# Kernel optimization log

Measured on AMD Instinct MI355X. Metric: run time of the kernel, lower is better.

The kernel has to match this reference:

```python
import jax, jax.numpy as jnp
import numpy as np

B, N, E, H = 2, 2048, 512, 8
D = E // H
SCALE_BASE = 512.0
EPS = 1e-6


def _xpos_tables(n, d):
    # XPOS (torchscale): per-dim scale ramp + standard sinusoidal freqs
    half = d // 2
    xscale = (np.arange(0, d, 2, dtype=np.float32) + 0.4 * d) / (1.4 * d)  # [half]
    min_pos = -(n // 2)
    power = (np.arange(min_pos, n + min_pos, dtype=np.float32) / SCALE_BASE)[:, None]
    scale = xscale[None, :] ** power                                       # [n, half]
    inv_freq = 1.0 / (10000.0 ** (np.arange(0, half, dtype=np.float32) / half))
    sinusoid = np.arange(n, dtype=np.float32)[:, None] * inv_freq[None, :]  # [n, half]
    return (jnp.asarray(np.sin(sinusoid), jnp.float32),
            jnp.asarray(np.cos(sinusoid), jnp.float32),
            jnp.asarray(scale, jnp.float32))


def _dup_interleave(m):
    # [n, half] -> [n, d], each column repeated twice interleaved
    return jnp.repeat(m, 2, axis=-1)


def _rotate_every_two(x):
    x1, x2 = x[..., ::2], x[..., 1::2]
    return jnp.stack((-x2, x1), axis=-1).reshape(x.shape)


def _apply_xpos(x, sin, cos, scale):
    s = _dup_interleave(sin * scale)  # [n, d]
    c = _dup_interleave(cos * scale)
    return x * c + _rotate_every_two(x) * s


def _decay_mask(n, dtype=jnp.float32):
    # gammas per head: 1 - exp(linspace(log(1/32), log(1/512), H))
    gammas = 1.0 - jnp.exp(jnp.linspace(np.log(1.0 / 32), np.log(1.0 / 512), H)).astype(dtype)
    pos = jnp.arange(n, dtype=dtype)
    dist = pos[:, None] - pos[None, :]                 # [n, s]
    dist_c = jnp.where(dist >= 0, dist, 0.0)
    return jnp.where(dist[None] >= 0, gammas[:, None, None] ** dist_c[None], 0.0)  # [h, n, s]


def _msr_forward(query, key, value, Wq, bq, Wk, bk, Wv, bv, Wg, bg, Wo, bo):
    b, n, e = query.shape
    q = (query @ Wq.T + bq).reshape(b, n, H, D).transpose(0, 2, 1, 3)  # [b,h,n,d]
    k = (key   @ Wk.T + bk).reshape(b, n, H, D).transpose(0, 2, 1, 3)
    v = (value @ Wv.T + bv).reshape(b, n, H, D).transpose(0, 2, 1, 3)

    sin, cos, scale = _xpos_tables(n, D)
    q = _apply_xpos(q, sin, cos, scale)
    k = _apply_xpos(k, sin, cos, 1.0 / scale)  # downscale=True

    k = k / jnp.asarray(np.sqrt(D), q.dtype)   # scale = head_dim ** 0.5
    mask = _decay_mask(n, q.dtype)             # [h,n,s]

    sim = jnp.einsum('bhnd,bhsd->bhns', q, k) * mask[None]
    ret = jnp.einsum('bhns,bhsd->bhnd', sim, v)  # [b,h,n,d]

    # GroupNorm(groups=H, channels=H, affine=False) on [(b n), h, d]:
    # normalize each (b, n, h) slice over its d elements
    mean = ret.mean(axis=-1, keepdims=True)
    var = ret.var(axis=-1, keepdims=True)
    ret = (ret - mean) / jnp.sqrt(var + EPS)

    ret = ret.transpose(0, 2, 1, 3).reshape(b, n, e)
    gate = jax.nn.silu(query @ Wg.T + bg)
    return (ret * gate) @ Wo.T + bo


def setup_inputs() -> dict:
    key = jax.random.key(0)
    ks = jax.random.split(key, 13)
    std = float(np.sqrt(2.0 / (E + E)))  # xavier_normal for square Linear
    mk = lambda k: jax.random.normal(k, (E, E), jnp.float32) * std
    return {
        'query': jax.random.normal(ks[0], (B, N, E), jnp.float32),
        'key':   jax.random.normal(ks[1], (B, N, E), jnp.float32),
        'value': jax.random.normal(ks[2], (B, N, E), jnp.float32),
        'Wq': mk(ks[3]), 'bq': jnp.zeros((E,), jnp.float32),
        'Wk': mk(ks[4]), 'bk': jnp.zeros((E,), jnp.float32),
        'Wv': mk(ks[5]), 'bv': jnp.zeros((E,), jnp.float32),
        'Wg': mk(ks[6]), 'bg': jnp.zeros((E,), jnp.float32),
        'Wo': mk(ks[7]), 'bo': jnp.zeros((E,), jnp.float32),
    }


def reference(query, key, value, Wq, bq, Wk, bk, Wv, bv, Wg, bg, Wo, bo):
    return _msr_forward(query, key, value, Wq, bq, Wk, bk, Wv, bv, Wg, bg, Wo, bo)
```

## Files before the change

kernel.cpp:

```cpp
#include <hip/hip_runtime.h>
#include <math.h>

#define Bc 2
#define Nc 2048
#define Ec 512
#define Hc 8
#define Dc 64
#define Mc 4096
#define NT 32
#define Cc 64

typedef short bf16x8 __attribute__((ext_vector_type(8)));
typedef float f32x4 __attribute__((ext_vector_type(4)));

#define GLOAD(g, l) __builtin_amdgcn_global_load_lds(                        \
    (const __attribute__((address_space(1))) unsigned*)(const void*)(g),     \
    (__attribute__((address_space(3))) unsigned*)(void*)(l), 16, 0, 0)

#define VMCNT(n) asm volatile("s_waitcnt vmcnt(" #n ")" ::: "memory")

__device__ __forceinline__ unsigned short f2bf(float x) {
    union { float f; unsigned u; } v; v.f = x;
    unsigned r = v.u + 0x7fffu + ((v.u >> 16) & 1u);
    return (unsigned short)(r >> 16);
}
__device__ __forceinline__ float bf2f(unsigned short b) {
    union { float f; unsigned u; } v; v.u = ((unsigned)b) << 16;
    return v.f;
}

__device__ __forceinline__ float get_gamma(int h) {
    const float l0 = -3.4657359028f;
    const float l1 = -6.2383246250f;
    return 1.0f - expf(l0 + (l1 - l0) * ((float)h / 7.0f));
}

struct SplitArgs {
    const float* src[8];
    unsigned short* hi[8];
    unsigned short* lo[8];
    int n[8];
};

__global__ __launch_bounds__(256) void prep_kernel(SplitArgs a,
                                                   float* __restrict__ sinS,
                                                   float* __restrict__ cosS,
                                                   float* __restrict__ sinIS,
                                                   float* __restrict__ cosIS) {
    int y = blockIdx.y;
    if (y == 8) {
        int idx = blockIdx.x * 256 + threadIdx.x;
        if (idx >= Nc * 32) return;
        int n = idx & 2047;
        int i = idx >> 11;
        float xscale = (2.0f * (float)i + 25.6f) / 89.6f;
        float power  = ((float)n - 1024.0f) / 512.0f;
        float scale  = powf(xscale, power);
        float inv_freq = powf(10000.0f, -(float)i / 32.0f);
        float ang = (float)n * inv_freq;
        float s = sinf(ang), c = cosf(ang);
        int o = i * 2048 + n;
        sinS[o]  = s * scale;
        cosS[o]  = c * scale;
        float rs = 0.125f / scale;
        sinIS[o] = s * rs;
        cosIS[o] = c * rs;
        return;
    }
    int i4 = (blockIdx.x * 256 + threadIdx.x) * 4;
    if (i4 >= a.n[y]) return;
    float4 v = *(const float4*)&a.src[y][i4];
    ushort4 h, l;
    h.x = f2bf(v.x); l.x = f2bf(v.x - bf2f(h.x));
    h.y = f2bf(v.y); l.y = f2bf(v.y - bf2f(h.y));
    h.z = f2bf(v.z); l.z = f2bf(v.z - bf2f(h.z));
    h.w = f2bf(v.w); l.w = f2bf(v.w - bf2f(h.w));
    *(ushort4*)&a.hi[y][i4] = h;
    *(ushort4*)&a.lo[y][i4] = l;
}

template<int TM, int TN, int WR, int WC>
__global__ __launch_bounds__(WR * WC * 64) void mgemm_kernel(
    const unsigned short* __restrict__ Xq_h, const unsigned short* __restrict__ Xq_l,
    const unsigned short* __restrict__ Xk_h, const unsigned short* __restrict__ Xk_l,
    const unsigned short* __restrict__ Xv_h, const unsigned short* __restrict__ Xv_l,
    const unsigned short* __restrict__ Xr_h, const unsigned short* __restrict__ Xr_l,
    const unsigned short* __restrict__ Wq_h, const unsigned short* __restrict__ Wq_l,
    const unsigned short* __restrict__ Wk_h, const unsigned short* __restrict__ Wk_l,
    const unsigned short* __restrict__ Wv_h, const unsigned short* __restrict__ Wv_l,
    const unsigned short* __restrict__ Wg_h, const unsigned short* __restrict__ Wg_l,
    const unsigned short* __restrict__ Wo_h, const unsigned short* __restrict__ Wo_l,
    const float* __restrict__ bq, const float* __restrict__ bk, const float* __restrict__ bv,
    const float* __restrict__ bg, const float* __restrict__ bo,
    float* __restrict__ Qr, float* __restrict__ Kr, float* __restrict__ Vr,
    float* __restrict__ G, float* __restrict__ Out,
    const float* __restrict__ sinS, const float* __restrict__ cosS,
    const float* __restrict__ sinIS, const float* __restrict__ cosIS,
    int mode_base)
{
    constexpr int THREADS = WR * WC * 64;
    constexpr int MI  = TM / WR / 16;
    constexpr int NI  = TN / WC / 16;
    constexpr int RA  = TM * 4 / THREADS;
    constexpr int RB  = TN * 4 / THREADS;
    constexpr int BUF = (TM + TN) * 64;
    constexpr int ALo = TM * 32;
    constexpr int BHo = TM * 64;
    constexpr int BLo = TM * 64 + TN * 32;
    constexpr int NSTEP = Ec / 32;
    static_assert(RA == 1 && RB == 2 && NI == 4, "phase schedule assumes this shape");

    int gx = gridDim.x, gy = gridDim.y;
    int nwg = gx * gy * gridDim.z;
    int id = blockIdx.x + gx * (blockIdx.y + gy * blockIdx.z);
    int sid = (id & 7) * (nwg >> 3) + (id >> 3);
    int bx = sid % gx; int rest = sid / gx;
    int by = rest % gy; int bz = rest / gy;

    int mode = mode_base + bz;
    const unsigned short *Xh, *Xl, *Wh, *Wl; const float* bias;
    switch (mode) {
        case 0:  Xh = Xq_h; Xl = Xq_l; Wh = Wq_h; Wl = Wq_l; bias = bq; break;
        case 1:  Xh = Xk_h; Xl = Xk_l; Wh = Wk_h; Wl = Wk_l; bias = bk; break;
        case 2:  Xh = Xv_h; Xl = Xv_l; Wh = Wv_h; Wl = Wv_l; bias = bv; break;
        case 3:  Xh = Xq_h; Xl = Xq_l; Wh = Wg_h; Wl = Wg_l; bias = bg; break;
        default: Xh = Xr_h; Xl = Xr_l; Wh = Wo_h; Wl = Wo_l; bias = bo; break;
    }

    __shared__ __align__(16) short lds[3 * BUF];

    int tid  = threadIdx.x;
    int lane = tid & 63;
    int w    = tid >> 6;
    int wr   = w / WC, wc = w % WC;
    int row0 = bx * TM, col0 = by * TN;
    int lrow = lane & 15, lslot = lane >> 4;

    f32x4 acc[MI][NI];
    #pragma unroll
    for (int i = 0; i < MI; ++i)
        #pragma unroll
        for (int j = 0; j < NI; ++j) acc[i][j] = {0.f, 0.f, 0.f, 0.f};

    int aoff[MI], boff[NI];
    #pragma unroll
    for (int mi = 0; mi < MI; ++mi) {
        int r = wr * (TM / WR) + mi * 16 + lrow;
        aoff[mi] = (r * 4 + (lslot ^ ((r >> 1) & 3))) * 8;
    }
    #pragma unroll
    for (int ni = 0; ni < NI; ++ni) {
        int r = wc * (TN / WC) + ni * 16 + lrow;
        boff[ni] = (r * 4 + (lslot ^ ((r >> 1) & 3))) * 8;
    }

    auto stage_full = [&](int buf, int k0) {
        short* l = &lds[buf * BUF];
        {
            int q = tid;
            int r = q >> 2;
            int sp = (q & 3) ^ ((r >> 1) & 3);
            int base = (w << 6) * 8;
            size_t ga = (size_t)(row0 + r) * Ec + k0 + sp * 8;
            GLOAD(Xh + ga, &l[base]);
            GLOAD(Xl + ga, &l[ALo + base]);
        }
        #pragma unroll
        for (int i = 0; i < RB; ++i) {
            int q = i * THREADS + tid;
            int r = q >> 2;
            int sp = (q & 3) ^ ((r >> 1) & 3);
            int base = (i * THREADS + (w << 6)) * 8;
            size_t gb = (size_t)(col0 + r) * Ec + k0 + sp * 8;
            GLOAD(Wh + gb, &l[BHo + base]);
            GLOAD(Wl + gb, &l[BLo + base]);
        }
    };
    auto stage_portion = [&](int buf, int k0, int p) {
        short* l = &lds[buf * BUF];
        if (p == 0) {
            int q = tid;
            int r = q >> 2;
            int sp = (q & 3) ^ ((r >> 1) & 3);
            int base = (w << 6) * 8;
            size_t ga = (size_t)(row0 + r) * Ec + k0 + sp * 8;
            GLOAD(Xh + ga, &l[base]);
            GLOAD(Xl + ga, &l[ALo + base]);
        } else if (p <= 2) {
            int i = p - 1;
            int q = i * THREADS + tid;
            int r = q >> 2;
            int sp = (q & 3) ^ ((r >> 1) & 3);
            int base = (i * THREADS + (w << 6)) * 8;
            size_t gb = (size_t)(col0 + r) * Ec + k0 + sp * 8;
            GLOAD(Wh + gb, &l[BHo + base]);
            GLOAD(Wl + gb, &l[BLo + base]);
        }
    };

    stage_full(0, 0);
    stage_full(1, 32);
    VMCNT(6);
    __builtin_amdgcn_s_barrier();

    bf16x8 ah[MI], al[MI];
    for (int t = 0; t < NSTEP; ++t) {
        const int cur = t % 3;
        const short* l = &lds[cur * BUF];
        const bool pre = (t + 2) < NSTEP;
        const int nb = (t + 2) % 3;
        const int nk = (t + 2) * 32;
        #pragma unroll
        for (int p = 0; p < 4; ++p) {
            if (p == 0) {
                #pragma unroll
                for (int mi = 0; mi < MI; ++mi) {
                    ah[mi] = *(const bf16x8*)&l[aoff[mi]];
                    al[mi] = *(const bf16x8*)&l[ALo + aoff[mi]];
                }
            }
            bf16x8 bh2 = *(const bf16x8*)&l[BHo + boff[p]];
            bf16x8 bl2 = *(const bf16x8*)&l[BLo + boff[p]];
            if (pre) stage_portion(nb, nk, p);
            __builtin_amdgcn_s_barrier();
            asm volatile("s_waitcnt lgkmcnt(0)" ::: "memory");
            __builtin_amdgcn_sched_barrier(0);
            __builtin_amdgcn_s_setprio(1);
            #pragma unroll
            for (int mi = 0; mi < MI; ++mi) {
                acc[mi][p] = __builtin_amdgcn_mfma_f32_16x16x32_bf16(ah[mi], bh2, acc[mi][p], 0, 0, 0);
                acc[mi][p] = __builtin_amdgcn_mfma_f32_16x16x32_bf16(ah[mi], bl2, acc[mi][p], 0, 0, 0);
                acc[mi][p] = __builtin_amdgcn_mfma_f32_16x16x32_bf16(al[mi], bh2, acc[mi][p], 0, 0, 0);
            }
            __builtin_amdgcn_s_setprio(0);
            if (p == 3) { if (pre) VMCNT(6); else VMCNT(0); }
            __builtin_amdgcn_s_barrier();
        }
    }

    int quad = lslot;
    if (mode <= 1) {
        const float* st = (mode == 0) ? sinS : sinIS;
        const float* ct = (mode == 0) ? cosS : cosIS;
        float* dst = (mode == 0) ? Qr : Kr;
        #pragma unroll
        for (int ni = 0; ni < NI; ++ni) {
            int c = col0 + wc * (TN / WC) + ni * 16 + lrow;
            int h = c >> 6, d = c & 63, pr = d >> 1;
            float bi = bias[c];
            #pragma unroll
            for (int mi = 0; mi < MI; ++mi) {
                int R0 = row0 + wr * (TM / WR) + mi * 16 + quad * 4;
                int bb = R0 >> 11;
                int n0 = R0 & 2047;
                float4 sv4 = *(const float4*)&st[pr * 2048 + n0];
                float4 cv4 = *(const float4*)&ct[pr * 2048 + n0];
                float svv[4] = {sv4.x, sv4.y, sv4.z, sv4.w};
                float cvv[4] = {cv4.x, cv4.y, cv4.z, cv4.w};
                #pragma unroll
                for (int reg = 0; reg < 4; ++reg) {
                    float x = acc[mi][ni][reg] + bi;
                    float p2 = __shfl_xor(x, 1, 64);
                    float y = (c & 1) ? fmaf(x, cvv[reg],  p2 * svv[reg])
                                      : fmaf(x, cvv[reg], -p2 * svv[reg]);
                    dst[(((size_t)(bb * Hc + h)) * Nc + n0 + reg) * Dc + d] = y;
                }
            }
        }
    } else if (mode == 2) {
        #pragma unroll
        for (int ni = 0; ni < NI; ++ni) {
            int c = col0 + wc * (TN / WC) + ni * 16 + lrow;
            int h = c >> 6, d = c & 63;
            float bi = bias[c];
            #pragma unroll
            for (int mi = 0; mi < MI; ++mi) {
                int R0 = row0 + wr * (TM / WR) + mi * 16 + quad * 4;
                int bb = R0 >> 11;
                int n0 = R0 & 2047;
                #pragma unroll
                for (int reg = 0; reg < 4; ++reg)
                    Vr[(((size_t)(bb * Hc + h)) * Nc + n0 + reg) * Dc + d] =
                        acc[mi][ni][reg] + bi;
            }
        }
    } else {
        #pragma unroll
        for (int ni = 0; ni < NI; ++ni) {
            int c = col0 + wc * (TN / WC) + ni * 16 + lrow;
            float bi = bias[c];
            #pragma unroll
            for (int mi = 0; mi < MI; ++mi) {
                int R0 = row0 + wr * (TM / WR) + mi * 16 + quad * 4;
                #pragma unroll
                for (int reg = 0; reg < 4; ++reg) {
                    float x = acc[mi][ni][reg] + bi;
                    if (mode == 3)
                        G[(size_t)(R0 + reg) * Ec + c] = x / (1.0f + expf(-x));
                    else
                        Out[(size_t)(R0 + reg) * Ec + c] = x;
                }
            }
        }
    }
}

__global__ __launch_bounds__(256) void phaseA_kernel(const float* __restrict__ Kr,
                                                     const float* __restrict__ Vr,
                                                     float* __restrict__ L)
{
    int bh = blockIdx.x;
    int t  = blockIdx.y;
    float gamma = get_gamma(bh & 7);
    float lg = logf(gamma);

    __shared__ float Ks[64][68];
    __shared__ float Vs[64][68];

    int tid = threadIdx.x;
    const float* Kc = Kr + (size_t)(bh * Nc + t * Cc) * Dc;
    const float* Vc = Vr + (size_t)(bh * Nc + t * Cc) * Dc;

    #pragma unroll
    for (int i = 0; i < 4; ++i) {
        int f = tid + i * 256;
        int s = f >> 4;
        int d = (f & 15) << 2;
        float w = expf(lg * (float)(Cc - s));
        float4 kv = *(const float4*)&Kc[s * Dc + d];
        float4 ks = {kv.x * w, kv.y * w, kv.z * w, kv.w * w};
        *(float4*)&Ks[s][d] = ks;
        float4 vv = *(const float4*)&Vc[s * Dc + d];
        *(float4*)&Vs[s][d] = vv;
    }
    __syncthreads();

    int tx = tid & 15, ty = tid >> 4;
    float acc[4][4];
    #pragma unroll
    for (int i = 0; i < 4; ++i)
        #pragma unroll
        for (int j = 0; j < 4; ++j) acc[i][j] = 0.0f;

    for (int s = 0; s < 64; ++s) {
        float4 a = *(const float4*)&Ks[s][ty * 4];
        float4 b = *(const float4*)&Vs[s][tx * 4];
        float av[4] = {a.x, a.y, a.z, a.w};
        float bv[4] = {b.x, b.y, b.z, b.w};
        #pragma unroll
        for (int i = 0; i < 4; ++i)
            #pragma unroll
            for (int j = 0; j < 4; ++j)
                acc[i][j] = fmaf(av[i], bv[j], acc[i][j]);
    }

    float* Lp = L + (size_t)(bh * NT + t) * 4096;
    #pragma unroll
    for (int i = 0; i < 4; ++i) {
        float4 o = {acc[i][0], acc[i][1], acc[i][2], acc[i][3]};
        *(float4*)&Lp[(ty * 4 + i) * 64 + tx * 4] = o;
    }
}

__global__ __launch_bounds__(256) void scan_kernel(const float* __restrict__ L,
                                                   float* __restrict__ Sst)
{
    int bh = blockIdx.x;
    int part = blockIdx.y;
    int tid = threadIdx.x;
    float gamma = get_gamma(bh & 7);
    float g64 = expf(logf(gamma) * 64.0f);

    float4 s = {0.0f, 0.0f, 0.0f, 0.0f};
    size_t base = (size_t)bh * NT * 4096 + part * 1024 + tid * 4;
    const float* Lp = L + base;
    float* Sp = Sst + base;
    for (int t = 0; t < NT; ++t) {
        *(float4*)&Sp[(size_t)t * 4096] = s;
        float4 l = *(const float4*)&Lp[(size_t)t * 4096];
        s.x = s.x * g64 + l.x;
        s.y = s.y * g64 + l.y;
        s.z = s.z * g64 + l.z;
        s.w = s.w * g64 + l.w;
    }
}

__global__ __launch_bounds__(256) void phaseC_kernel(
    const float* __restrict__ Qr, const float* __restrict__ Kr, const float* __restrict__ Vr,
    const float* __restrict__ Sst, const float* __restrict__ G,
    unsigned short* __restrict__ retGh, unsigned short* __restrict__ retGl)
{
    int bh = blockIdx.x, t = blockIdx.y;
    int b = bh >> 3, h = bh & 7;
    float gamma = get_gamma(h);
    float lg = logf(gamma);

    __shared__ float QsT[64][68];
    __shared__ float KsT[64][68];
    __shared__ float Ss[64][68];

    int tid = threadIdx.x;
    const float* Qc = Qr + (size_t)(bh * Nc + t * Cc) * Dc;
    const float* Kc = Kr + (size_t)(bh * Nc + t * Cc) * Dc;
    const float* Sp = Sst + (size_t)(bh * NT + t) * 4096;

    #pragma unroll
    for (int i = 0; i < 4; ++i) {
        int f = tid + i * 256;
        int r = f >> 4;
        int d = (f & 15) << 2;
        float wq = expf(lg * (float)r);
        float4 q = *(const float4*)&Qc[r * Dc + d];
        QsT[d + 0][r] = q.x * wq; QsT[d + 1][r] = q.y * wq;
        QsT[d + 2][r] = q.z * wq; QsT[d + 3][r] = q.w * wq;
        float wk = expf(-lg * (float)r);
        float4 kk = *(const float4*)&Kc[r * Dc + d];
        KsT[d + 0][r] = kk.x * wk; KsT[d + 1][r] = kk.y * wk;
        KsT[d + 2][r] = kk.z * wk; KsT[d + 3][r] = kk.w * wk;
        float4 sv = *(const float4*)&Sp[r * 64 + d];
        *(float4*)&Ss[r][d] = sv;
    }
    __syncthreads();

    int tx = tid & 15, ty = tid >> 4;
    float accA[4][4], accO[4][4];
    #pragma unroll
    for (int i = 0; i < 4; ++i)
        #pragma unroll
        for (int j = 0; j < 4; ++j) { accA[i][j] = 0.0f; accO[i][j] = 0.0f; }

    for (int d = 0; d < 64; ++d) {
        float4 a  = *(const float4*)&QsT[d][ty * 4];
        float4 kb = *(const float4*)&KsT[d][tx * 4];
        float4 sb = *(const float4*)&Ss[d][tx * 4];
        float av[4] = {a.x, a.y, a.z, a.w};
        float kv[4] = {kb.x, kb.y, kb.z, kb.w};
        float sv[4] = {sb.x, sb.y, sb.z, sb.w};
        #pragma unroll
        for (int i = 0; i < 4; ++i)
            #pragma unroll
            for (int j = 0; j < 4; ++j) {
                accA[i][j] = fmaf(av[i], kv[j], accA[i][j]);
                accO[i][j] = fmaf(av[i], sv[j], accO[i][j]);
            }
    }
    __syncthreads();

    #pragma unroll
    for (int i = 0; i < 4; ++i) {
        int gi = ty * 4 + i;
        #pragma unroll
        for (int j = 0; j < 4; ++j) {
            int gj = tx * 4 + j;
            KsT[gj][gi] = (gj <= gi) ? accA[i][j] : 0.0f;
        }
    }
    const float* Vc = Vr + (size_t)(bh * Nc + t * Cc) * Dc;
    #pragma unroll
    for (int i = 0; i < 4; ++i) {
        int f = tid + i * 256;
        int r = f >> 4;
        int d = (f & 15) << 2;
        float4 vv = *(const float4*)&Vc[r * Dc + d];
        *(float4*)&QsT[r][d] = vv;
    }
    __syncthreads();

    for (int j = 0; j < 64; ++j) {
        float4 a = *(const float4*)&KsT[j][ty * 4];
        float4 v = *(const float4*)&QsT[j][tx * 4];
        float av[4] = {a.x, a.y, a.z, a.w};
        float vv[4] = {v.x, v.y, v.z, v.w};
        #pragma unroll
        for (int i = 0; i < 4; ++i)
            #pragma unroll
            for (int jj = 0; jj < 4; ++jj)
                accO[i][jj] = fmaf(av[i], vv[jj], accO[i][jj]);
    }

    #pragma unroll
    for (int i = 0; i < 4; ++i) {
        float sum = accO[i][0] + accO[i][1] + accO[i][2] + accO[i][3];
        float sq  = accO[i][0] * accO[i][0] + accO[i][1] * accO[i][1]
                  + accO[i][2] * accO[i][2] + accO[i][3] * accO[i][3];
        #pragma unroll
        for (int m = 1; m < 16; m <<= 1) {
            sum += __shfl_xor(sum, m, 64);
            sq  += __shfl_xor(sq,  m, 64);
        }
        float mean = sum * (1.0f / 64.0f);
        float var  = sq * (1.0f / 64.0f) - mean * mean;
        float rinv = rsqrtf(var + 1e-6f);
        #pragma unroll
        for (int jj = 0; jj < 4; ++jj)
            accO[i][jj] = (accO[i][jj] - mean) * rinv;
    }

    #pragma unroll
    for (int i = 0; i < 4; ++i) {
        int n = t * Cc + ty * 4 + i;
        size_t idx = ((size_t)b * Nc + n) * Ec + h * Dc + tx * 4;
        float4 g = *(const float4*)&G[idx];
        float o0 = accO[i][0] * g.x, o1 = accO[i][1] * g.y;
        float o2 = accO[i][2] * g.z, o3 = accO[i][3] * g.w;
        ushort4 hh, ll;
        hh.x = f2bf(o0); ll.x = f2bf(o0 - bf2f(hh.x));
        hh.y = f2bf(o1); ll.y = f2bf(o1 - bf2f(hh.y));
        hh.z = f2bf(o2); ll.z = f2bf(o2 - bf2f(hh.z));
        hh.w = f2bf(o3); ll.w = f2bf(o3 - bf2f(hh.w));
        *(ushort4*)&retGh[idx] = hh;
        *(ushort4*)&retGl[idx] = ll;
    }
}

extern "C" void kernel_launch(void* const* d_in, const int* in_sizes, int n_in,
                              void* d_out, int out_size, void* d_ws, size_t ws_size,
                              hipStream_t stream) {
    const float* query = (const float*)d_in[0];
    const float* key   = (const float*)d_in[1];
    const float* value = (const float*)d_in[2];
    const float* Wq = (const float*)d_in[3];
    const float* bq = (const float*)d_in[4];
    const float* Wk = (const float*)d_in[5];
    const float* bk = (const float*)d_in[6];
    const float* Wv = (const float*)d_in[7];
    const float* bv = (const float*)d_in[8];
    const float* Wg = (const float*)d_in[9];
    const float* bg = (const float*)d_in[10];
    const float* Wo = (const float*)d_in[11];
    const float* bo = (const float*)d_in[12];
    float* out = (float*)d_out;

    float* wsf = (float*)d_ws;
    const size_t SZ = (size_t)Bc * Nc * Ec;

    float* Qr = wsf;
    float* Kr = Qr + SZ;
    float* Vr = Kr + SZ;
    float* G  = Vr + SZ;

    unsigned short* Xq_h = (unsigned short*)(wsf + 4 * SZ);
    unsigned short* Xq_l = Xq_h + SZ;
    unsigned short* Xk_h = Xq_l + SZ;
    unsigned short* Xk_l = Xk_h + SZ;
    unsigned short* Xv_h = Xk_l + SZ;
    unsigned short* Xv_l = Xv_h + SZ;
    float* L   = wsf + 4 * SZ;
    float* Sst = wsf + 5 * SZ;
    unsigned short* retGh = (unsigned short*)(wsf + 6 * SZ);
    unsigned short* retGl = retGh + SZ;

    const size_t WSZ = (size_t)Ec * Ec;
    unsigned short* Wp = (unsigned short*)(wsf + 7 * SZ);
    unsigned short* Wq_h = Wp;            unsigned short* Wq_l = Wp + WSZ;
    unsigned short* Wk_h = Wp + 2 * WSZ;  unsigned short* Wk_l = Wp + 3 * WSZ;
    unsigned short* Wv_h = Wp + 4 * WSZ;  unsigned short* Wv_l = Wp + 5 * WSZ;
    unsigned short* Wg_h = Wp + 6 * WSZ;  unsigned short* Wg_l = Wp + 7 * WSZ;
    unsigned short* Wo_h = Wp + 8 * WSZ;  unsigned short* Wo_l = Wp + 9 * WSZ;

    float* tab = wsf + 7 * SZ + (10 * WSZ) / 2;
    float* sinS  = tab;
    float* cosS  = sinS + Nc * 32;
    float* sinIS = cosS + Nc * 32;
    float* cosIS = sinIS + Nc * 32;

    SplitArgs sa;
    sa.src[0] = query; sa.hi[0] = Xq_h; sa.lo[0] = Xq_l; sa.n[0] = (int)SZ;
    sa.src[1] = key;   sa.hi[1] = Xk_h; sa.lo[1] = Xk_l; sa.n[1] = (int)SZ;
    sa.src[2] = value; sa.hi[2] = Xv_h; sa.lo[2] = Xv_l; sa.n[2] = (int)SZ;
    sa.src[3] = Wq;    sa.hi[3] = Wq_h; sa.lo[3] = Wq_l; sa.n[3] = (int)WSZ;
    sa.src[4] = Wk;    sa.hi[4] = Wk_h; sa.lo[4] = Wk_l; sa.n[4] = (int)WSZ;
    sa.src[5] = Wv;    sa.hi[5] = Wv_h; sa.lo[5] = Wv_l; sa.n[5] = (int)WSZ;
    sa.src[6] = Wg;    sa.hi[6] = Wg_h; sa.lo[6] = Wg_l; sa.n[6] = (int)WSZ;
    sa.src[7] = Wo;    sa.hi[7] = Wo_h; sa.lo[7] = Wo_l; sa.n[7] = (int)WSZ;
    prep_kernel<<<dim3(2048, 9), dim3(256), 0, stream>>>(sa, sinS, cosS, sinIS, cosIS);

    mgemm_kernel<128, 256, 2, 4><<<dim3(Mc / 128, Ec / 256, 4), dim3(512), 0, stream>>>(
        Xq_h, Xq_l, Xk_h, Xk_l, Xv_h, Xv_l, retGh, retGl,
        Wq_h, Wq_l, Wk_h, Wk_l, Wv_h, Wv_l, Wg_h, Wg_l, Wo_h, Wo_l,
        bq, bk, bv, bg, bo, Qr, Kr, Vr, G, out,
        sinS, cosS, sinIS, cosIS, 0);

    phaseA_kernel<<<dim3(Bc * Hc, NT), dim3(256), 0, stream>>>(Kr, Vr, L);
    scan_kernel<<<dim3(Bc * Hc, 4), dim3(256), 0, stream>>>(L, Sst);
    phaseC_kernel<<<dim3(Bc * Hc, NT), dim3(256), 0, stream>>>(Qr, Kr, Vr, Sst, G, retGh, retGl);

    mgemm_kernel<64, 128, 2, 2><<<dim3(Mc / 64, Ec / 128, 1), dim3(256), 0, stream>>>(
        Xq_h, Xq_l, Xk_h, Xk_l, Xv_h, Xv_l, retGh, retGl,
        Wq_h, Wq_l, Wk_h, Wk_l, Wv_h, Wv_l, Wg_h, Wg_l, Wo_h, Wo_l,
        bq, bk, bv, bg, bo, Qr, Kr, Vr, G, out,
        sinS, cosS, sinIS, cosIS, 4);
}
```

Measured before the change: 178.1 us.

## Split projection GEMM into double-buffered 128x128 kernel and dedicated output GEMM

The fused QKVG projection GEMM moves from a 128x256 tile with triple-buffered, phase-interleaved staging to a 128x128 tile with plain double buffering, where each k-step loads all fragments before issuing the MFMAs. This gives more workgroups for better CU fill and a simpler schedule. The cost is less data reuse per tile and less overlap between loads and compute. The output projection gets its own specialised kernel without mode dispatch, and the scan kernel now uses 64-thread blocks with four times as many blocks to spread the work.

```diff
diff --git a/kernel.cpp b/kernel.cpp
--- a/kernel.cpp
+++ b/kernel.cpp
@@ -79,166 +79,14 @@
     *(ushort4*)&a.lo[y][i4] = l;
 }
 
-template<int TM, int TN, int WR, int WC>
-__global__ __launch_bounds__(WR * WC * 64) void mgemm_kernel(
-    const unsigned short* __restrict__ Xq_h, const unsigned short* __restrict__ Xq_l,
-    const unsigned short* __restrict__ Xk_h, const unsigned short* __restrict__ Xk_l,
-    const unsigned short* __restrict__ Xv_h, const unsigned short* __restrict__ Xv_l,
-    const unsigned short* __restrict__ Xr_h, const unsigned short* __restrict__ Xr_l,
-    const unsigned short* __restrict__ Wq_h, const unsigned short* __restrict__ Wq_l,
-    const unsigned short* __restrict__ Wk_h, const unsigned short* __restrict__ Wk_l,
-    const unsigned short* __restrict__ Wv_h, const unsigned short* __restrict__ Wv_l,
-    const unsigned short* __restrict__ Wg_h, const unsigned short* __restrict__ Wg_l,
-    const unsigned short* __restrict__ Wo_h, const unsigned short* __restrict__ Wo_l,
-    const float* __restrict__ bq, const float* __restrict__ bk, const float* __restrict__ bv,
-    const float* __restrict__ bg, const float* __restrict__ bo,
-    float* __restrict__ Qr, float* __restrict__ Kr, float* __restrict__ Vr,
-    float* __restrict__ G, float* __restrict__ Out,
-    const float* __restrict__ sinS, const float* __restrict__ cosS,
-    const float* __restrict__ sinIS, const float* __restrict__ cosIS,
-    int mode_base)
+template<int TM, int TN, int WR, int WC, int MI, int NI>
+__device__ __forceinline__ void gemm_epilogue(
+    f32x4 (&acc)[MI][NI], int mode, int row0, int col0, int wr, int wc,
+    int lrow, int quad, const float* bias,
+    float* Qr, float* Kr, float* Vr, float* G, float* Out,
+    const float* sinS, const float* cosS,
+    const float* sinIS, const float* cosIS)
 {
-    constexpr int THREADS = WR * WC * 64;
-    constexpr int MI  = TM / WR / 16;
-    constexpr int NI  = TN / WC / 16;
-    constexpr int RA  = TM * 4 / THREADS;
-    constexpr int RB  = TN * 4 / THREADS;
-    constexpr int BUF = (TM + TN) * 64;
-    constexpr int ALo = TM * 32;
-    constexpr int BHo = TM * 64;
-    constexpr int BLo = TM * 64 + TN * 32;
-    constexpr int NSTEP = Ec / 32;
-    static_assert(RA == 1 && RB == 2 && NI == 4, "phase schedule assumes this shape");
-
-    int gx = gridDim.x, gy = gridDim.y;
-    int nwg = gx * gy * gridDim.z;
-    int id = blockIdx.x + gx * (blockIdx.y + gy * blockIdx.z);
-    int sid = (id & 7) * (nwg >> 3) + (id >> 3);
-    int bx = sid % gx; int rest = sid / gx;
-    int by = rest % gy; int bz = rest / gy;
-
-    int mode = mode_base + bz;
-    const unsigned short *Xh, *Xl, *Wh, *Wl; const float* bias;
-    switch (mode) {
-        case 0:  Xh = Xq_h; Xl = Xq_l; Wh = Wq_h; Wl = Wq_l; bias = bq; break;
-        case 1:  Xh = Xk_h; Xl = Xk_l; Wh = Wk_h; Wl = Wk_l; bias = bk; break;
-        case 2:  Xh = Xv_h; Xl = Xv_l; Wh = Wv_h; Wl = Wv_l; bias = bv; break;
-        case 3:  Xh = Xq_h; Xl = Xq_l; Wh = Wg_h; Wl = Wg_l; bias = bg; break;
-        default: Xh = Xr_h; Xl = Xr_l; Wh = Wo_h; Wl = Wo_l; bias = bo; break;
-    }
-
-    __shared__ __align__(16) short lds[3 * BUF];
-
-    int tid  = threadIdx.x;
-    int lane = tid & 63;
-    int w    = tid >> 6;
-    int wr   = w / WC, wc = w % WC;
-    int row0 = bx * TM, col0 = by * TN;
-    int lrow = lane & 15, lslot = lane >> 4;
-
-    f32x4 acc[MI][NI];
-    #pragma unroll
-    for (int i = 0; i < MI; ++i)
-        #pragma unroll
-        for (int j = 0; j < NI; ++j) acc[i][j] = {0.f, 0.f, 0.f, 0.f};
-
-    int aoff[MI], boff[NI];
-    #pragma unroll
-    for (int mi = 0; mi < MI; ++mi) {
-        int r = wr * (TM / WR) + mi * 16 + lrow;
-        aoff[mi] = (r * 4 + (lslot ^ ((r >> 1) & 3))) * 8;
-    }
-    #pragma unroll
-    for (int ni = 0; ni < NI; ++ni) {
-        int r = wc * (TN / WC) + ni * 16 + lrow;
-        boff[ni] = (r * 4 + (lslot ^ ((r >> 1) & 3))) * 8;
-    }
-
-    auto stage_full = [&](int buf, int k0) {
-        short* l = &lds[buf * BUF];
-        {
-            int q = tid;
-            int r = q >> 2;
-            int sp = (q & 3) ^ ((r >> 1) & 3);
-            int base = (w << 6) * 8;
-            size_t ga = (size_t)(row0 + r) * Ec + k0 + sp * 8;
-            GLOAD(Xh + ga, &l[base]);
-            GLOAD(Xl + ga, &l[ALo + base]);
-        }
-        #pragma unroll
-        for (int i = 0; i < RB; ++i) {
-            int q = i * THREADS + tid;
-            int r = q >> 2;
-            int sp = (q & 3) ^ ((r >> 1) & 3);
-            int base = (i * THREADS + (w << 6)) * 8;
-            size_t gb = (size_t)(col0 + r) * Ec + k0 + sp * 8;
-            GLOAD(Wh + gb, &l[BHo + base]);
-            GLOAD(Wl + gb, &l[BLo + base]);
-        }
-    };
-    auto stage_portion = [&](int buf, int k0, int p) {
-        short* l = &lds[buf * BUF];
-        if (p == 0) {
-            int q = tid;
-            int r = q >> 2;
-            int sp = (q & 3) ^ ((r >> 1) & 3);
-            int base = (w << 6) * 8;
-            size_t ga = (size_t)(row0 + r) * Ec + k0 + sp * 8;
-            GLOAD(Xh + ga, &l[base]);
-            GLOAD(Xl + ga, &l[ALo + base]);
-        } else if (p <= 2) {
-            int i = p - 1;
-            int q = i * THREADS + tid;
-            int r = q >> 2;
-            int sp = (q & 3) ^ ((r >> 1) & 3);
-            int base = (i * THREADS + (w << 6)) * 8;
-            size_t gb = (size_t)(col0 + r) * Ec + k0 + sp * 8;
-            GLOAD(Wh + gb, &l[BHo + base]);
-            GLOAD(Wl + gb, &l[BLo + base]);
-        }
-    };
-
-    stage_full(0, 0);
-    stage_full(1, 32);
-    VMCNT(6);
-    __builtin_amdgcn_s_barrier();
-
-    bf16x8 ah[MI], al[MI];
-    for (int t = 0; t < NSTEP; ++t) {
-        const int cur = t % 3;
-        const short* l = &lds[cur * BUF];
-        const bool pre = (t + 2) < NSTEP;
-        const int nb = (t + 2) % 3;
-        const int nk = (t + 2) * 32;
-        #pragma unroll
-        for (int p = 0; p < 4; ++p) {
-            if (p == 0) {
-                #pragma unroll
-                for (int mi = 0; mi < MI; ++mi) {
-                    ah[mi] = *(const bf16x8*)&l[aoff[mi]];
-                    al[mi] = *(const bf16x8*)&l[ALo + aoff[mi]];
-                }
-            }
-            bf16x8 bh2 = *(const bf16x8*)&l[BHo + boff[p]];
-            bf16x8 bl2 = *(const bf16x8*)&l[BLo + boff[p]];
-            if (pre) stage_portion(nb, nk, p);
-            __builtin_amdgcn_s_barrier();
-            asm volatile("s_waitcnt lgkmcnt(0)" ::: "memory");
-            __builtin_amdgcn_sched_barrier(0);
-            __builtin_amdgcn_s_setprio(1);
-            #pragma unroll
-            for (int mi = 0; mi < MI; ++mi) {
-                acc[mi][p] = __builtin_amdgcn_mfma_f32_16x16x32_bf16(ah[mi], bh2, acc[mi][p], 0, 0, 0);
-                acc[mi][p] = __builtin_amdgcn_mfma_f32_16x16x32_bf16(ah[mi], bl2, acc[mi][p], 0, 0, 0);
-                acc[mi][p] = __builtin_amdgcn_mfma_f32_16x16x32_bf16(al[mi], bh2, acc[mi][p], 0, 0, 0);
-            }
-            __builtin_amdgcn_s_setprio(0);
-            if (p == 3) { if (pre) VMCNT(6); else VMCNT(0); }
-            __builtin_amdgcn_s_barrier();
-        }
-    }
-
-    int quad = lslot;
     if (mode <= 1) {
         const float* st = (mode == 0) ? sinS : sinIS;
         const float* ct = (mode == 0) ? cosS : cosIS;
@@ -305,6 +153,293 @@
     }
 }
 
+template<int TM, int TN, int WR, int WC>
+__global__ __launch_bounds__(WR * WC * 64) void mgemm2_kernel(
+    const unsigned short* __restrict__ Xq_h, const unsigned short* __restrict__ Xq_l,
+    const unsigned short* __restrict__ Xk_h, const unsigned short* __restrict__ Xk_l,
+    const unsigned short* __restrict__ Xv_h, const unsigned short* __restrict__ Xv_l,
+    const unsigned short* __restrict__ Wq_h, const unsigned short* __restrict__ Wq_l,
+    const unsigned short* __restrict__ Wk_h, const unsigned short* __restrict__ Wk_l,
+    const unsigned short* __restrict__ Wv_h, const unsigned short* __restrict__ Wv_l,
+    const unsigned short* __restrict__ Wg_h, const unsigned short* __restrict__ Wg_l,
+    const float* __restrict__ bq, const float* __restrict__ bk, const float* __restrict__ bv,
+    const float* __restrict__ bg,
+    float* __restrict__ Qr, float* __restrict__ Kr, float* __restrict__ Vr,
+    float* __restrict__ G,
+    const float* __restrict__ sinS, const float* __restrict__ cosS,
+    const float* __restrict__ sinIS, const float* __restrict__ cosIS)
+{
+    constexpr int THREADS = WR * WC * 64;
+    constexpr int MI  = TM / WR / 16;
+    constexpr int NI  = TN / WC / 16;
+    constexpr int RA  = TM * 4 / THREADS;
+    constexpr int RB  = TN * 4 / THREADS;
+    constexpr int GL  = 2 * (RA + RB);
+    constexpr int BUF = (TM + TN) * 64;
+    constexpr int ALo = TM * 32;
+    constexpr int BHo = TM * 64;
+    constexpr int BLo = TM * 64 + TN * 32;
+    static_assert(GL == 8, "vmcnt literal");
+
+    int gx = gridDim.x, gy = gridDim.y;
+    int nwg = gx * gy * gridDim.z;
+    int id = blockIdx.x + gx * (blockIdx.y + gy * blockIdx.z);
+    int sid = (id & 7) * (nwg >> 3) + (id >> 3);
+    int bx = sid % gx; int rest = sid / gx;
+    int by = rest % gy; int bz = rest / gy;
+
+    int mode = bz;
+    const unsigned short *Xh, *Xl, *Wh, *Wl; const float* bias;
+    switch (mode) {
+        case 0:  Xh = Xq_h; Xl = Xq_l; Wh = Wq_h; Wl = Wq_l; bias = bq; break;
+        case 1:  Xh = Xk_h; Xl = Xk_l; Wh = Wk_h; Wl = Wk_l; bias = bk; break;
+        case 2:  Xh = Xv_h; Xl = Xv_l; Wh = Wv_h; Wl = Wv_l; bias = bv; break;
+        default: Xh = Xq_h; Xl = Xq_l; Wh = Wg_h; Wl = Wg_l; bias = bg; break;
+    }
+
+    __shared__ __align__(16) short lds[2 * BUF];
+
+    int tid  = threadIdx.x;
+    int lane = tid & 63;
+    int w    = tid >> 6;
+    int wr   = w / WC, wc = w % WC;
+    int row0 = bx * TM, col0 = by * TN;
+    int lrow = lane & 15, lslot = lane >> 4;
+
+    f32x4 acc[MI][NI];
+    #pragma unroll
+    for (int i = 0; i < MI; ++i)
+        #pragma unroll
+        for (int j = 0; j < NI; ++j) acc[i][j] = {0.f, 0.f, 0.f, 0.f};
+
+    int aoff[MI], boff[NI];
+    #pragma unroll
+    for (int mi = 0; mi < MI; ++mi) {
+        int r = wr * (TM / WR) + mi * 16 + lrow;
+        aoff[mi] = (r * 4 + (lslot ^ ((r >> 1) & 3))) * 8;
+    }
+    #pragma unroll
+    for (int ni = 0; ni < NI; ++ni) {
+        int r = wc * (TN / WC) + ni * 16 + lrow;
+        boff[ni] = (r * 4 + (lslot ^ ((r >> 1) & 3))) * 8;
+    }
+
+    auto stage = [&](int buf, int k0) {
+        short* l = &lds[buf * BUF];
+        #pragma unroll
+        for (int i = 0; i < RA; ++i) {
+            int q = i * THREADS + tid;
+            int r = q >> 2;
+            int sp = (q & 3) ^ ((r >> 1) & 3);
+            int base = (i * THREADS + (w << 6)) * 8;
+            size_t ga = (size_t)(row0 + r) * Ec + k0 + sp * 8;
+            GLOAD(Xh + ga, &l[base]);
+            GLOAD(Xl + ga, &l[ALo + base]);
+        }
+        #pragma unroll
+        for (int i = 0; i < RB; ++i) {
+            int q = i * THREADS + tid;
+            int r = q >> 2;
+            int sp = (q & 3) ^ ((r >> 1) & 3);
+            int base = (i * THREADS + (w << 6)) * 8;
+            size_t gb = (size_t)(col0 + r) * Ec + k0 + sp * 8;
+            GLOAD(Wh + gb, &l[BHo + base]);
+            GLOAD(Wl + gb, &l[BLo + base]);
+        }
+    };
+
+    stage(0, 0);
+    for (int t = 0; t < Ec / 32; ++t) {
+        int cur = t & 1;
+        if (t < Ec / 32 - 1) {
+            stage(cur ^ 1, (t + 1) * 32);
+            VMCNT(8);
+        } else {
+            VMCNT(0);
+        }
+        __builtin_amdgcn_s_barrier();
+        __builtin_amdgcn_sched_barrier(0);
+
+        const short* l = &lds[cur * BUF];
+        bf16x8 ah[MI], al[MI], bh[NI], bl[NI];
+        #pragma unroll
+        for (int mi = 0; mi < MI; ++mi) {
+            ah[mi] = *(const bf16x8*)&l[aoff[mi]];
+            al[mi] = *(const bf16x8*)&l[ALo + aoff[mi]];
+        }
+        #pragma unroll
+        for (int ni = 0; ni < NI; ++ni) {
+            bh[ni] = *(const bf16x8*)&l[BHo + boff[ni]];
+            bl[ni] = *(const bf16x8*)&l[BLo + boff[ni]];
+        }
+        #pragma unroll
+        for (int mi = 0; mi < MI; ++mi)
+            #pragma unroll
+            for (int ni = 0; ni < NI; ++ni) {
+                acc[mi][ni] = __builtin_amdgcn_mfma_f32_16x16x32_bf16(ah[mi], bh[ni], acc[mi][ni], 0, 0, 0);
+                acc[mi][ni] = __builtin_amdgcn_mfma_f32_16x16x32_bf16(ah[mi], bl[ni], acc[mi][ni], 0, 0, 0);
+                acc[mi][ni] = __builtin_amdgcn_mfma_f32_16x16x32_bf16(al[mi], bh[ni], acc[mi][ni], 0, 0, 0);
+            }
+        asm volatile("s_waitcnt lgkmcnt(0)" ::: "memory");
+        __builtin_amdgcn_sched_barrier(0);
+        __builtin_amdgcn_s_barrier();
+    }
+
+    gemm_epilogue<TM, TN, WR, WC, MI, NI>(acc, mode, row0, col0, wr, wc,
+        lrow, lslot, bias, Qr, Kr, Vr, G, (float*)nullptr,
+        sinS, cosS, sinIS, cosIS);
+}
+
+template<int TM, int TN, int WR, int WC>
+__global__ __launch_bounds__(WR * WC * 64) void mgemm4_kernel(
+    const unsigned short* __restrict__ Xr_h, const unsigned short* __restrict__ Xr_l,
+    const unsigned short* __restrict__ Wo_h, const unsigned short* __restrict__ Wo_l,
+    const float* __restrict__ bo, float* __restrict__ Out)
+{
+    constexpr int THREADS = WR * WC * 64;
+    constexpr int MI  = TM / WR / 16;
+    constexpr int NI  = TN / WC / 16;
+    constexpr int RA  = TM * 4 / THREADS;
+    constexpr int RB  = TN * 4 / THREADS;
+    constexpr int BUF = (TM + TN) * 64;
+    constexpr int ALo = TM * 32;
+    constexpr int BHo = TM * 64;
+    constexpr int BLo = TM * 64 + TN * 32;
+    constexpr int NSTEP = Ec / 32;
+    static_assert(RA == 1 && RB == 2 && NI == 4, "phase schedule assumes this shape");
+
+    int gx = gridDim.x;
+    int nwg = gx * gridDim.y;
+    int id = blockIdx.x + gx * blockIdx.y;
+    int sid = (id & 7) * (nwg >> 3) + (id >> 3);
+    int bx = sid % gx; int by = sid / gx;
+
+    __shared__ __align__(16) short lds[3 * BUF];
+
+    int tid  = threadIdx.x;
+    int lane = tid & 63;
+    int w    = tid >> 6;
+    int wr   = w / WC, wc = w % WC;
+    int row0 = bx * TM, col0 = by * TN;
+    int lrow = lane & 15, lslot = lane >> 4;
+
+    f32x4 acc[MI][NI];
+    #pragma unroll
+    for (int i = 0; i < MI; ++i)
+        #pragma unroll
+        for (int j = 0; j < NI; ++j) acc[i][j] = {0.f, 0.f, 0.f, 0.f};
+
+    int aoff[MI], boff[NI];
+    #pragma unroll
+    for (int mi = 0; mi < MI; ++mi) {
+        int r = wr * (TM / WR) + mi * 16 + lrow;
+        aoff[mi] = (r * 4 + (lslot ^ ((r >> 1) & 3))) * 8;
+    }
+    #pragma unroll
+    for (int ni = 0; ni < NI; ++ni) {
+        int r = wc * (TN / WC) + ni * 16 + lrow;
+        boff[ni] = (r * 4 + (lslot ^ ((r >> 1) & 3))) * 8;
+    }
+
+    auto stage_full = [&](int buf, int k0) {
+        short* l = &lds[buf * BUF];
+        {
+            int q = tid;
+            int r = q >> 2;
+            int sp = (q & 3) ^ ((r >> 1) & 3);
+            int base = (w << 6) * 8;
+            size_t ga = (size_t)(row0 + r) * Ec + k0 + sp * 8;
+            GLOAD(Xr_h + ga, &l[base]);
+            GLOAD(Xr_l + ga, &l[ALo + base]);
+        }
+        #pragma unroll
+        for (int i = 0; i < RB; ++i) {
+            int q = i * THREADS + tid;
+            int r = q >> 2;
+            int sp = (q & 3) ^ ((r >> 1) & 3);
+            int base = (i * THREADS + (w << 6)) * 8;
+            size_t gb = (size_t)(col0 + r) * Ec + k0 + sp * 8;
+            GLOAD(Wo_h + gb, &l[BHo + base]);
+            GLOAD(Wo_l + gb, &l[BLo + base]);
+        }
+    };
+    auto stage_portion = [&](int buf, int k0, int p) {
+        short* l = &lds[buf * BUF];
+        if (p == 0) {
+            int q = tid;
+            int r = q >> 2;
+            int sp = (q & 3) ^ ((r >> 1) & 3);
+            int base = (w << 6) * 8;
+            size_t ga = (size_t)(row0 + r) * Ec + k0 + sp * 8;
+            GLOAD(Xr_h + ga, &l[base]);
+            GLOAD(Xr_l + ga, &l[ALo + base]);
+        } else if (p <= 2) {
+            int i = p - 1;
+            int q = i * THREADS + tid;
+            int r = q >> 2;
+            int sp = (q & 3) ^ ((r >> 1) & 3);
+            int base = (i * THREADS + (w << 6)) * 8;
+            size_t gb = (size_t)(col0 + r) * Ec + k0 + sp * 8;
+            GLOAD(Wo_h + gb, &l[BHo + base]);
+            GLOAD(Wo_l + gb, &l[BLo + base]);
+        }
+    };
+
+    stage_full(0, 0);
+    stage_full(1, 32);
+    VMCNT(6);
+    __builtin_amdgcn_s_barrier();
+
+    bf16x8 ah[MI], al[MI];
+    for (int t = 0; t < NSTEP; ++t) {
+        const int cur = t % 3;
+        const short* l = &lds[cur * BUF];
+        const bool pre = (t + 2) < NSTEP;
+        const int nb = (t + 2) % 3;
+        const int nk = (t + 2) * 32;
+        #pragma unroll
+        for (int p = 0; p < 4; ++p) {
+            if (p == 0) {
+                #pragma unroll
+                for (int mi = 0; mi < MI; ++mi) {
+                    ah[mi] = *(const bf16x8*)&l[aoff[mi]];
+                    al[mi] = *(const bf16x8*)&l[ALo + aoff[mi]];
+                }
+            }
+            bf16x8 bh2 = *(const bf16x8*)&l[BHo + boff[p]];
+            bf16x8 bl2 = *(const bf16x8*)&l[BLo + boff[p]];
+            if (pre) stage_portion(nb, nk, p);
+            __builtin_amdgcn_s_barrier();
+            asm volatile("s_waitcnt lgkmcnt(0)" ::: "memory");
+            __builtin_amdgcn_sched_barrier(0);
+            __builtin_amdgcn_s_setprio(1);
+            #pragma unroll
+            for (int mi = 0; mi < MI; ++mi) {
+                acc[mi][p] = __builtin_amdgcn_mfma_f32_16x16x32_bf16(ah[mi], bh2, acc[mi][p], 0, 0, 0);
+                acc[mi][p] = __builtin_amdgcn_mfma_f32_16x16x32_bf16(ah[mi], bl2, acc[mi][p], 0, 0, 0);
+                acc[mi][p] = __builtin_amdgcn_mfma_f32_16x16x32_bf16(al[mi], bh2, acc[mi][p], 0, 0, 0);
+            }
+            __builtin_amdgcn_s_setprio(0);
+            if (p == 3) { if (pre) VMCNT(6); else VMCNT(0); }
+            __builtin_amdgcn_s_barrier();
+        }
+    }
+
+    int quad = lslot;
+    #pragma unroll
+    for (int ni = 0; ni < NI; ++ni) {
+        int c = col0 + wc * (TN / WC) + ni * 16 + lrow;
+        float bi = bo[c];
+        #pragma unroll
+        for (int mi = 0; mi < MI; ++mi) {
+            int R0 = row0 + wr * (TM / WR) + mi * 16 + quad * 4;
+            #pragma unroll
+            for (int reg = 0; reg < 4; ++reg)
+                Out[(size_t)(R0 + reg) * Ec + c] = acc[mi][ni][reg] + bi;
+        }
+    }
+}
+
 __global__ __launch_bounds__(256) void phaseA_kernel(const float* __restrict__ Kr,
                                                      const float* __restrict__ Vr,
                                                      float* __restrict__ L)
@@ -362,8 +497,8 @@
     }
 }
 
-__global__ __launch_bounds__(256) void scan_kernel(const float* __restrict__ L,
-                                                   float* __restrict__ Sst)
+__global__ __launch_bounds__(64) void scan_kernel(const float* __restrict__ L,
+                                                  float* __restrict__ Sst)
 {
     int bh = blockIdx.x;
     int part = blockIdx.y;
@@ -372,7 +507,7 @@
     float g64 = expf(logf(gamma) * 64.0f);
 
     float4 s = {0.0f, 0.0f, 0.0f, 0.0f};
-    size_t base = (size_t)bh * NT * 4096 + part * 1024 + tid * 4;
+    size_t base = (size_t)bh * NT * 4096 + part * 256 + tid * 4;
     const float* Lp = L + base;
     float* Sp = Sst + base;
     for (int t = 0; t < NT; ++t) {
@@ -575,19 +710,16 @@
     sa.src[7] = Wo;    sa.hi[7] = Wo_h; sa.lo[7] = Wo_l; sa.n[7] = (int)WSZ;
     prep_kernel<<<dim3(2048, 9), dim3(256), 0, stream>>>(sa, sinS, cosS, sinIS, cosIS);
 
-    mgemm_kernel<128, 256, 2, 4><<<dim3(Mc / 128, Ec / 256, 4), dim3(512), 0, stream>>>(
-        Xq_h, Xq_l, Xk_h, Xk_l, Xv_h, Xv_l, retGh, retGl,
-        Wq_h, Wq_l, Wk_h, Wk_l, Wv_h, Wv_l, Wg_h, Wg_l, Wo_h, Wo_l,
-        bq, bk, bv, bg, bo, Qr, Kr, Vr, G, out,
-        sinS, cosS, sinIS, cosIS, 0);
+    mgemm2_kernel<128, 128, 2, 2><<<dim3(Mc / 128, Ec / 128, 4), dim3(256), 0, stream>>>(
+        Xq_h, Xq_l, Xk_h, Xk_l, Xv_h, Xv_l,
+        Wq_h, Wq_l, Wk_h, Wk_l, Wv_h, Wv_l, Wg_h, Wg_l,
+        bq, bk, bv, bg, Qr, Kr, Vr, G,
+        sinS, cosS, sinIS, cosIS);
 
     phaseA_kernel<<<dim3(Bc * Hc, NT), dim3(256), 0, stream>>>(Kr, Vr, L);
-    scan_kernel<<<dim3(Bc * Hc, 4), dim3(256), 0, stream>>>(L, Sst);
+    scan_kernel<<<dim3(Bc * Hc, 16), dim3(64), 0, stream>>>(L, Sst);
     phaseC_kernel<<<dim3(Bc * Hc, NT), dim3(256), 0, stream>>>(Qr, Kr, Vr, Sst, G, retGh, retGl);
 
-    mgemm_kernel<64, 128, 2, 2><<<dim3(Mc / 64, Ec / 128, 1), dim3(256), 0, stream>>>(
-        Xq_h, Xq_l, Xk_h, Xk_l, Xv_h, Xv_l, retGh, retGl,
-        Wq_h, Wq_l, Wk_h, Wk_l, Wv_h, Wv_l, Wg_h, Wg_l, Wo_h, Wo_l,
-        bq, bk, bv, bg, bo, Qr, Kr, Vr, G, out,
-        sinS, cosS, sinIS, cosIS, 4);
-}
+    mgemm4_kernel<64, 128, 2, 2><<<dim3(Mc / 64, Ec / 128), dim3(256), 0, stream>>>(
+        retGh, retGl, Wo_h, Wo_l, bo, out);
+}
```

Result: no change. 180.9 us (+1.6%).
